# Optimization experiments

Hardware: AMD Instinct MI355X
Metric: run time of the kernel (lower is better)

The kernel has to match this reference:

```python
import jax, jax.numpy as jnp
import numpy as np

N_NODES = 50000
N_EDGES = 800000
F_IN, F_HID, F_OUT = 128, 64, 32


def setup_inputs() -> dict:
    key = jax.random.key(0)
    k1, k2, k3, k4, k5, k6 = jax.random.split(key, 6)
    x = jax.random.normal(k1, (N_NODES, F_IN), dtype=jnp.float32)
    edge_index = jax.random.randint(k2, (2, N_EDGES), 0, N_NODES, dtype=jnp.int64)
    # Glorot-ish init for the two GCNConv linear layers
    W1 = jax.random.normal(k3, (F_IN, F_HID), dtype=jnp.float32) / np.sqrt(F_IN)
    b1 = jnp.zeros((F_HID,), dtype=jnp.float32)
    W2 = jax.random.normal(k4, (F_HID, F_OUT), dtype=jnp.float32) / np.sqrt(F_HID)
    b2 = jnp.zeros((F_OUT,), dtype=jnp.float32)
    return {"x": x, "edge_index": edge_index, "W1": W1, "b1": b1, "W2": W2, "b2": b2}


def _gcn_conv(x, src, dst, norm, W, b):
    # GCNConv: linear transform, then D^{-1/2}(A+I)D^{-1/2} aggregation
    xw = x @ W                                # [N, F_out]
    msg = xw[src] * norm[:, None]             # [E+N, F_out] gather + scale
    out = jax.ops.segment_sum(msg, dst, num_segments=x.shape[0])
    return out + b


def reference(x, edge_index, W1, b1, W2, b2):
    n = x.shape[0]
    self_loops = jnp.arange(n, dtype=edge_index.dtype)
    src = jnp.concatenate([edge_index[0], self_loops])  # [E+N]
    dst = jnp.concatenate([edge_index[1], self_loops])
    # symmetric degree normalization (self-loops guarantee deg >= 1)
    deg = jax.ops.segment_sum(jnp.ones_like(dst, dtype=x.dtype), dst, num_segments=n)
    dinv = jax.lax.rsqrt(deg)
    norm = dinv[src] * dinv[dst]              # [E+N]

    h = _gcn_conv(x, src, dst, norm, W1, b1)
    h = jax.nn.relu(h)
    # dropout p=0.5 is identity in eval mode (training=False)
    out = _gcn_conv(h, src, dst, norm, W2, b2)
    return out
```

## Files before the change

kernel.cpp:

```cpp
#include <hip/hip_runtime.h>
#include <hip/hip_fp16.h>

#define NN 50000
#define NE 800000
#define F_IN 128
#define F_HID 64
#define F_OUT 32
#define CAP 48
#define NPB 196
#define EPB 4096
#define NB2 391
#define CELL 40
#define NXW1 782

typedef _Float16 f16x8 __attribute__((ext_vector_type(8)));
typedef float f32x4 __attribute__((ext_vector_type(4)));
#define XS_STR 136


__global__ __launch_bounds__(256) void fused_xw1_partition_kernel(
        const float* __restrict__ x, const float* __restrict__ W,
        const int* __restrict__ src, const int* __restrict__ dst,
        int* __restrict__ cnt2t, unsigned int* __restrict__ bstore2,
        __half* __restrict__ outh) {
    __shared__ _Float16 xs[64 * XS_STR];
    __shared__ _Float16 wt[64 * XS_STR];
    __shared__ int hist[4][NB2];
    __shared__ int cur[NB2];
    int t = threadIdx.x;

    if (blockIdx.x < NPB) {
        int blk = blockIdx.x;
        for (int i = t; i < 4 * NB2; i += 256) ((int*)hist)[i] = 0;
        __syncthreads();
        int wv = t >> 6;
        int base = blk * EPB;
        unsigned int pk[16];
#pragma unroll
        for (int i = 0; i < 16; ++i) {
            int e = base + i * 256 + t;
            if (e < NE) {
                unsigned int d = (unsigned int)dst[e];
                unsigned int s = (unsigned int)src[e];
                pk[i] = (d << 16) | s;
                atomicAdd(&hist[wv][d >> 7], 1);
            } else {
                pk[i] = 0xFFFFFFFFu;
            }
        }
        __syncthreads();
        for (int b = t; b < NB2; b += 256) {
            int h = hist[0][b] + hist[1][b] + hist[2][b] + hist[3][b];
            cur[b] = 0;
            cnt2t[b * NPB + blk] = h;
        }
        __syncthreads();
#pragma unroll
        for (int i = 0; i < 16; ++i) {
            unsigned int p = pk[i];
            if (p != 0xFFFFFFFFu) {
                int b = p >> 23;
                int pos = atomicAdd(&cur[b], 1);
                if (pos < CELL) bstore2[((size_t)blk * NB2 + b) * CELL + pos] = p;
            }
        }
        return;
    }

    int node0 = (blockIdx.x - NPB) * 64;

    {
        int r = t >> 2;
        int c0 = (t & 3) * 32;
        int gn = node0 + r;
        if (gn > NN - 1) gn = NN - 1;
        const float4* xrow = (const float4*)(x + (size_t)gn * F_IN);
#pragma unroll
        for (int i = 0; i < 8; ++i) {
            float4 v = xrow[(c0 >> 2) + i];
            _Float16* p = &xs[r * XS_STR + c0 + i * 4];
            p[0] = (_Float16)v.x; p[1] = (_Float16)v.y;
            p[2] = (_Float16)v.z; p[3] = (_Float16)v.w;
        }
    }
#pragma unroll
    for (int i = 0; i < 8; ++i) {
        int idx4 = t + i * 256;
        int k = idx4 >> 4;
        int n0 = (idx4 & 15) << 2;
        float4 v = ((const float4*)W)[idx4];
        wt[(n0 + 0) * XS_STR + k] = (_Float16)v.x;
        wt[(n0 + 1) * XS_STR + k] = (_Float16)v.y;
        wt[(n0 + 2) * XS_STR + k] = (_Float16)v.z;
        wt[(n0 + 3) * XS_STR + k] = (_Float16)v.w;
    }
    __syncthreads();

    int wave = t >> 6;
    int l = t & 63;
    int quad = l >> 4;
    int lm = l & 15;

    f32x4 acc[4] = {{0,0,0,0},{0,0,0,0},{0,0,0,0},{0,0,0,0}};
    const _Float16* abase = &xs[(wave * 16 + lm) * XS_STR + quad * 8];
#pragma unroll
    for (int kk4 = 0; kk4 < 4; ++kk4) {
        int kk = kk4 * 32;
        f16x8 a = *(const f16x8*)(abase + kk);
#pragma unroll
        for (int ft = 0; ft < 4; ++ft) {
            f16x8 b = *(const f16x8*)&wt[(ft * 16 + lm) * XS_STR + kk + quad * 8];
            acc[ft] = __builtin_amdgcn_mfma_f32_16x16x32_f16(a, b, acc[ft], 0, 0, 0);
        }
    }

    __syncthreads();
    _Float16* ot = xs;
#pragma unroll
    for (int ft = 0; ft < 4; ++ft) {
#pragma unroll
        for (int r = 0; r < 4; ++r) {
            int row_l = wave * 16 + quad * 4 + r;
            ot[row_l * 64 + ft * 16 + lm] = (_Float16)acc[ft][r];
        }
    }
    __syncthreads();
#pragma unroll
    for (int i = 0; i < 2; ++i) {
        int idx = t + i * 256;
        int row = idx >> 3;
        int c8 = (idx & 7) * 8;
        int gn = node0 + row;
        if (gn < NN)
            *(uint4*)(outh + (size_t)gn * 64 + c8) = *(const uint4*)&ot[row * 64 + c8];
    }
}


__device__ __forceinline__ void slot_insert(unsigned int p, int* cnt_l,
                                            unsigned short* slot_l) {
    int dl = (p >> 16) & 127;
    int pos = atomicAdd(&cnt_l[dl], 1);
    if (pos < CAP) slot_l[dl * CAP + pos] = (unsigned short)(p & 0xFFFFu);
}

__global__ __launch_bounds__(256) void build_slots_kernel(
        const int* __restrict__ cnt2t, const unsigned int* __restrict__ bstore2,
        unsigned short* __restrict__ slot, int* __restrict__ cnt_g, float* __restrict__ dinv) {
    __shared__ unsigned short slot_l[128 * CAP];
    __shared__ int cnt_l[128];
    int t = threadIdx.x;
    int b = blockIdx.x;
    if (t < 128) cnt_l[t] = 0;
    __syncthreads();

    if (t < NPB) {
        int blk = t;
        int c = cnt2t[b * NPB + blk];
        if (c > CELL) c = CELL;
        const uint4* seg4 = (const uint4*)(bstore2 + ((size_t)blk * NB2 + b) * CELL);
        int c4 = c >> 2;
        for (int q = 0; q < c4; ++q) {
            uint4 u = seg4[q];
            slot_insert(u.x, cnt_l, slot_l);
            slot_insert(u.y, cnt_l, slot_l);
            slot_insert(u.z, cnt_l, slot_l);
            slot_insert(u.w, cnt_l, slot_l);
        }
        const unsigned int* seg = (const unsigned int*)seg4;
        for (int j = c4 * 4; j < c; ++j) slot_insert(seg[j], cnt_l, slot_l);
    }
    __syncthreads();

    unsigned int* sg = (unsigned int*)(slot + (size_t)b * 128 * CAP);
    const unsigned int* sl = (const unsigned int*)slot_l;
    for (int j = t; j < 128 * CAP / 2; j += 256) sg[j] = sl[j];

    if (t < 128) {
        int n = b * 128 + t;
        if (n < NN) {
            int c = cnt_l[t];
            cnt_g[n] = c;
            dinv[n] = rsqrtf(1.0f + (float)c);
        }
    }
}


__global__ __launch_bounds__(256, 6) void gather64_w2_kernel(
        const __half* __restrict__ xw, const int* __restrict__ cnt,
        const unsigned short* __restrict__ slot, const float* __restrict__ dinv,
        const float* __restrict__ b1, const float* __restrict__ W2,
        __half* __restrict__ hw2h) {
    __shared__ float w2s[F_HID * F_OUT];
    __shared__ float hl[4][F_HID];
    int t = threadIdx.x;
    for (int i = t; i < F_HID * F_OUT / 4; i += 256)
        ((float4*)w2s)[i] = ((const float4*)W2)[i];
    __syncthreads();

    int lane = t & 63;
    int wv = t >> 6;
    int n = blockIdx.x * 4 + wv;
    int st = lane >> 4;
    int fl4 = lane & 15;
    const uint2* base = (const uint2*)xw;
    int deg = cnt[n];
    if (deg > CAP) deg = CAP;
    float din = dinv[n];
    const unsigned short* srow = slot + (size_t)n * CAP;
    uint2 u_self = base[(size_t)n * 16 + fl4];
    float4 bb = ((const float4*)b1)[fl4];
    float a0 = 0, a1 = 0, a2 = 0, a3 = 0;
    int e = st;
    for (; e + 12 < deg; e += 16) {
        int s0 = srow[e];
        int s1 = srow[e + 4];
        int s2 = srow[e + 8];
        int s3 = srow[e + 12];
        float dv0 = dinv[s0], dv1 = dinv[s1], dv2 = dinv[s2], dv3 = dinv[s3];
        uint2 u0 = base[(size_t)s0 * 16 + fl4];
        uint2 u1 = base[(size_t)s1 * 16 + fl4];
        uint2 u2 = base[(size_t)s2 * 16 + fl4];
        uint2 u3 = base[(size_t)s3 * 16 + fl4];
        float2 p0 = __half22float2(*(__half2*)&u0.x), p1 = __half22float2(*(__half2*)&u0.y);
        float2 q0 = __half22float2(*(__half2*)&u1.x), q1 = __half22float2(*(__half2*)&u1.y);
        float2 r0 = __half22float2(*(__half2*)&u2.x), r1 = __half22float2(*(__half2*)&u2.y);
        float2 t0 = __half22float2(*(__half2*)&u3.x), t1 = __half22float2(*(__half2*)&u3.y);
        a0 += dv0 * p0.x + dv1 * q0.x + dv2 * r0.x + dv3 * t0.x;
        a1 += dv0 * p0.y + dv1 * q0.y + dv2 * r0.y + dv3 * t0.y;
        a2 += dv0 * p1.x + dv1 * q1.x + dv2 * r1.x + dv3 * t1.x;
        a3 += dv0 * p1.y + dv1 * q1.y + dv2 * r1.y + dv3 * t1.y;
    }
    for (; e < deg; e += 4) {
        int s = srow[e];
        float dv = dinv[s];
        uint2 u = base[(size_t)s * 16 + fl4];
        float2 p0 = __half22float2(*(__half2*)&u.x);
        float2 p1 = __half22float2(*(__half2*)&u.y);
        a0 += dv * p0.x; a1 += dv * p0.y; a2 += dv * p1.x; a3 += dv * p1.y;
    }
    a0 += __shfl_xor(a0, 16, 64); a1 += __shfl_xor(a1, 16, 64);
    a2 += __shfl_xor(a2, 16, 64); a3 += __shfl_xor(a3, 16, 64);
    a0 += __shfl_xor(a0, 32, 64); a1 += __shfl_xor(a1, 32, 64);
    a2 += __shfl_xor(a2, 32, 64); a3 += __shfl_xor(a3, 32, 64);
    if (st == 0) {
        float2 s0 = __half22float2(*(__half2*)&u_self.x);
        float2 s1 = __half22float2(*(__half2*)&u_self.y);
        float v0 = din * (a0 + din * s0.x) + bb.x;
        float v1 = din * (a1 + din * s0.y) + bb.y;
        float v2 = din * (a2 + din * s1.x) + bb.z;
        float v3 = din * (a3 + din * s1.y) + bb.w;
        float* hr = &hl[wv][fl4 * 4];
        hr[0] = v0 > 0.f ? v0 : 0.f;
        hr[1] = v1 > 0.f ? v1 : 0.f;
        hr[2] = v2 > 0.f ? v2 : 0.f;
        hr[3] = v3 > 0.f ? v3 : 0.f;
    }
    asm volatile("s_waitcnt lgkmcnt(0)" ::: "memory");
    {
        int f = lane & 31;
        int kh = lane >> 5;
        const float* hr = &hl[wv][kh * 32];
        float acc = 0.0f;
#pragma unroll
        for (int k = 0; k < 32; ++k) acc += hr[k] * w2s[(kh * 32 + k) * F_OUT + f];
        acc += __shfl_xor(acc, 32, 64);
        if (kh == 0) hw2h[(size_t)n * F_OUT + f] = __float2half(acc * din);
    }
}


__global__ __launch_bounds__(256, 8) void gather32_kernel(
        const __half* __restrict__ scaled, const int* __restrict__ cnt,
        const unsigned short* __restrict__ slot, const float* __restrict__ dinv,
        const float* __restrict__ bias, float* __restrict__ out) {
    int lane = threadIdx.x & 63;
    int n = blockIdx.x * 4 + (threadIdx.x >> 6);
    if (n >= NN) return;
    int st = lane >> 3;
    int fl4 = lane & 7;
    const uint2* base = (const uint2*)scaled;
    int deg = cnt[n];
    if (deg > CAP) deg = CAP;
    const unsigned short* srow = slot + (size_t)n * CAP;
    uint2 u_self = base[(size_t)n * 8 + fl4];
    float4 b4 = ((const float4*)bias)[fl4];
    float a0 = 0, a1 = 0, a2 = 0, a3 = 0;
    int e = st;
    for (; e + 8 < deg; e += 16) {
        int s0 = srow[e];
        int s1 = srow[e + 8];
        uint2 u0 = base[(size_t)s0 * 8 + fl4];
        uint2 u1 = base[(size_t)s1 * 8 + fl4];
        float2 p0 = __half22float2(*(__half2*)&u0.x);
        float2 p1 = __half22float2(*(__half2*)&u0.y);
        float2 q0 = __half22float2(*(__half2*)&u1.x);
        float2 q1 = __half22float2(*(__half2*)&u1.y);
        a0 += p0.x + q0.x; a1 += p0.y + q0.y;
        a2 += p1.x + q1.x; a3 += p1.y + q1.y;
    }
    for (; e < deg; e += 8) {
        int s = srow[e];
        uint2 u = base[(size_t)s * 8 + fl4];
        float2 p0 = __half22float2(*(__half2*)&u.x);
        float2 p1 = __half22float2(*(__half2*)&u.y);
        a0 += p0.x; a1 += p0.y; a2 += p1.x; a3 += p1.y;
    }
    a0 += __shfl_xor(a0, 8, 64);  a1 += __shfl_xor(a1, 8, 64);
    a2 += __shfl_xor(a2, 8, 64);  a3 += __shfl_xor(a3, 8, 64);
    a0 += __shfl_xor(a0, 16, 64); a1 += __shfl_xor(a1, 16, 64);
    a2 += __shfl_xor(a2, 16, 64); a3 += __shfl_xor(a3, 16, 64);
    a0 += __shfl_xor(a0, 32, 64); a1 += __shfl_xor(a1, 32, 64);
    a2 += __shfl_xor(a2, 32, 64); a3 += __shfl_xor(a3, 32, 64);
    if (st == 0) {
        float2 s0 = __half22float2(*(__half2*)&u_self.x);
        float2 s1 = __half22float2(*(__half2*)&u_self.y);
        float di = dinv[n];
        float4 r;
        r.x = di * (a0 + s0.x) + b4.x;
        r.y = di * (a1 + s0.y) + b4.y;
        r.z = di * (a2 + s1.x) + b4.z;
        r.w = di * (a3 + s1.y) + b4.w;
        ((float4*)out)[(size_t)n * 8 + fl4] = r;
    }
}


extern "C" void kernel_launch(void* const* d_in, const int* in_sizes, int n_in,
                              void* d_out, int out_size, void* d_ws, size_t ws_size,
                              hipStream_t stream) {
    const float* x  = (const float*)d_in[0];
    const int*   ei = (const int*)d_in[1];
    const float* W1 = (const float*)d_in[2];
    const float* b1 = (const float*)d_in[3];
    const float* W2 = (const float*)d_in[4];
    const float* b2 = (const float*)d_in[5];
    const int* src = ei;
    const int* dst = ei + NE;

    float*          ws      = (float*)d_ws;
    float*          dinv    = ws;
    int*            cnt     = (int*)(ws + 50048);
    int*            cnt2t   = (int*)(ws + 100096);
    unsigned int*   bstore2 = (unsigned int*)(ws + 176768);
    unsigned short* slot    = (unsigned short*)(ws + 3242208);
    __half*         xw1h    = (__half*)(ws + 4443360);
    __half*         hw2h    = (__half*)(ws + 6043360);
    float*          out     = (float*)d_out;

    fused_xw1_partition_kernel<<<NPB + NXW1, 256, 0, stream>>>(
        x, W1, src, dst, cnt2t, bstore2, xw1h);
    build_slots_kernel<<<NB2, 256, 0, stream>>>(cnt2t, bstore2, slot, cnt, dinv);
    gather64_w2_kernel<<<NN / 4, 256, 0, stream>>>(xw1h, cnt, slot, dinv, b1, W2, hw2h);
    gather32_kernel<<<NN / 4, 256, 0, stream>>>(hw2h, cnt, slot, dinv, b2, out);
}
```

Measured before the change: 149.1 us.

## Move X·W1 GEMM into slot-building kernel and hoist gather loads ahead of degree

The dense X·W1 GEMM blocks now launch alongside the slot-building blocks instead of the partition blocks, so the partition kernel becomes a small standalone launch. Both layers' gather kernels issue their first batch of neighbour indices and feature loads before reading the degree. They then mask out-of-range lanes, unrolling two fixed rounds before a remainder loop. This aims to raise memory-level parallelism and shorten dependency chains, at the cost of speculative reads of unused slot entries and a shared-memory union in the fused kernel.

```diff
diff --git a/kernel.cpp b/kernel.cpp
--- a/kernel.cpp
+++ b/kernel.cpp
@@ -18,56 +18,108 @@
 #define XS_STR 136
 
 
-__global__ __launch_bounds__(256) void fused_xw1_partition_kernel(
-        const float* __restrict__ x, const float* __restrict__ W,
+__global__ __launch_bounds__(256) void partition_kernel(
         const int* __restrict__ src, const int* __restrict__ dst,
-        int* __restrict__ cnt2t, unsigned int* __restrict__ bstore2,
-        __half* __restrict__ outh) {
-    __shared__ _Float16 xs[64 * XS_STR];
-    __shared__ _Float16 wt[64 * XS_STR];
+        int* __restrict__ cnt2t, unsigned int* __restrict__ bstore2) {
     __shared__ int hist[4][NB2];
     __shared__ int cur[NB2];
     int t = threadIdx.x;
-
-    if (blockIdx.x < NPB) {
-        int blk = blockIdx.x;
-        for (int i = t; i < 4 * NB2; i += 256) ((int*)hist)[i] = 0;
+    int blk = blockIdx.x;
+    for (int i = t; i < 4 * NB2; i += 256) ((int*)hist)[i] = 0;
+    __syncthreads();
+    int wv = t >> 6;
+    int base = blk * EPB;
+    unsigned int pk[16];
+#pragma unroll
+    for (int i = 0; i < 16; ++i) {
+        int e = base + i * 256 + t;
+        if (e < NE) {
+            unsigned int d = (unsigned int)dst[e];
+            unsigned int s = (unsigned int)src[e];
+            pk[i] = (d << 16) | s;
+            atomicAdd(&hist[wv][d >> 7], 1);
+        } else {
+            pk[i] = 0xFFFFFFFFu;
+        }
+    }
+    __syncthreads();
+    for (int b = t; b < NB2; b += 256) {
+        int h = hist[0][b] + hist[1][b] + hist[2][b] + hist[3][b];
+        cur[b] = 0;
+        cnt2t[b * NPB + blk] = h;
+    }
+    __syncthreads();
+#pragma unroll
+    for (int i = 0; i < 16; ++i) {
+        unsigned int p = pk[i];
+        if (p != 0xFFFFFFFFu) {
+            int b = p >> 23;
+            int pos = atomicAdd(&cur[b], 1);
+            if (pos < CELL) bstore2[((size_t)blk * NB2 + b) * CELL + pos] = p;
+        }
+    }
+}
+
+
+__device__ __forceinline__ void slot_insert(unsigned int p, int* cnt_l,
+                                            unsigned short* slot_l) {
+    int dl = (p >> 16) & 127;
+    int pos = atomicAdd(&cnt_l[dl], 1);
+    if (pos < CAP) slot_l[dl * CAP + pos] = (unsigned short)(p & 0xFFFFu);
+}
+
+__global__ __launch_bounds__(256) void fused_slots_xw1_kernel(
+        const int* __restrict__ cnt2t, const unsigned int* __restrict__ bstore2,
+        unsigned short* __restrict__ slot, int* __restrict__ cnt_g,
+        float* __restrict__ dinv,
+        const float* __restrict__ x, const float* __restrict__ W,
+        __half* __restrict__ outh) {
+    __shared__ __align__(16) char smem[64 * XS_STR * 2 * sizeof(_Float16)];
+    int t = threadIdx.x;
+
+    if (blockIdx.x < NB2) {
+        unsigned short* slot_l = (unsigned short*)smem;
+        int* cnt_l = (int*)(smem + 128 * CAP * sizeof(unsigned short));
+        int b = blockIdx.x;
+        if (t < 128) cnt_l[t] = 0;
         __syncthreads();
-        int wv = t >> 6;
-        int base = blk * EPB;
-        unsigned int pk[16];
-#pragma unroll
-        for (int i = 0; i < 16; ++i) {
-            int e = base + i * 256 + t;
-            if (e < NE) {
-                unsigned int d = (unsigned int)dst[e];
-                unsigned int s = (unsigned int)src[e];
-                pk[i] = (d << 16) | s;
-                atomicAdd(&hist[wv][d >> 7], 1);
-            } else {
-                pk[i] = 0xFFFFFFFFu;
+
+        if (t < NPB) {
+            int blk = t;
+            int c = cnt2t[b * NPB + blk];
+            if (c > CELL) c = CELL;
+            const uint4* seg4 = (const uint4*)(bstore2 + ((size_t)blk * NB2 + b) * CELL);
+            int c4 = c >> 2;
+            for (int q = 0; q < c4; ++q) {
+                uint4 u = seg4[q];
+                slot_insert(u.x, cnt_l, slot_l);
+                slot_insert(u.y, cnt_l, slot_l);
+                slot_insert(u.z, cnt_l, slot_l);
+                slot_insert(u.w, cnt_l, slot_l);
             }
+            const unsigned int* seg = (const unsigned int*)seg4;
+            for (int j = c4 * 4; j < c; ++j) slot_insert(seg[j], cnt_l, slot_l);
         }
         __syncthreads();
-        for (int b = t; b < NB2; b += 256) {
-            int h = hist[0][b] + hist[1][b] + hist[2][b] + hist[3][b];
-            cur[b] = 0;
-            cnt2t[b * NPB + blk] = h;
-        }
-        __syncthreads();
-#pragma unroll
-        for (int i = 0; i < 16; ++i) {
-            unsigned int p = pk[i];
-            if (p != 0xFFFFFFFFu) {
-                int b = p >> 23;
-                int pos = atomicAdd(&cur[b], 1);
-                if (pos < CELL) bstore2[((size_t)blk * NB2 + b) * CELL + pos] = p;
+
+        unsigned int* sg = (unsigned int*)(slot + (size_t)b * 128 * CAP);
+        const unsigned int* sl = (const unsigned int*)slot_l;
+        for (int j = t; j < 128 * CAP / 2; j += 256) sg[j] = sl[j];
+
+        if (t < 128) {
+            int n = b * 128 + t;
+            if (n < NN) {
+                int c = cnt_l[t];
+                cnt_g[n] = c;
+                dinv[n] = rsqrtf(1.0f + (float)c);
             }
         }
         return;
     }
 
-    int node0 = (blockIdx.x - NPB) * 64;
+    _Float16* xs = (_Float16*)smem;
+    _Float16* wt = xs + 64 * XS_STR;
+    int node0 = (blockIdx.x - NB2) * 64;
 
     {
         int r = t >> 2;
@@ -133,56 +185,6 @@
         int gn = node0 + row;
         if (gn < NN)
             *(uint4*)(outh + (size_t)gn * 64 + c8) = *(const uint4*)&ot[row * 64 + c8];
-    }
-}
-
-
-__device__ __forceinline__ void slot_insert(unsigned int p, int* cnt_l,
-                                            unsigned short* slot_l) {
-    int dl = (p >> 16) & 127;
-    int pos = atomicAdd(&cnt_l[dl], 1);
-    if (pos < CAP) slot_l[dl * CAP + pos] = (unsigned short)(p & 0xFFFFu);
-}
-
-__global__ __launch_bounds__(256) void build_slots_kernel(
-        const int* __restrict__ cnt2t, const unsigned int* __restrict__ bstore2,
-        unsigned short* __restrict__ slot, int* __restrict__ cnt_g, float* __restrict__ dinv) {
-    __shared__ unsigned short slot_l[128 * CAP];
-    __shared__ int cnt_l[128];
-    int t = threadIdx.x;
-    int b = blockIdx.x;
-    if (t < 128) cnt_l[t] = 0;
-    __syncthreads();
-
-    if (t < NPB) {
-        int blk = t;
-        int c = cnt2t[b * NPB + blk];
-        if (c > CELL) c = CELL;
-        const uint4* seg4 = (const uint4*)(bstore2 + ((size_t)blk * NB2 + b) * CELL);
-        int c4 = c >> 2;
-        for (int q = 0; q < c4; ++q) {
-            uint4 u = seg4[q];
-            slot_insert(u.x, cnt_l, slot_l);
-            slot_insert(u.y, cnt_l, slot_l);
-            slot_insert(u.z, cnt_l, slot_l);
-            slot_insert(u.w, cnt_l, slot_l);
-        }
-        const unsigned int* seg = (const unsigned int*)seg4;
-        for (int j = c4 * 4; j < c; ++j) slot_insert(seg[j], cnt_l, slot_l);
-    }
-    __syncthreads();
-
-    unsigned int* sg = (unsigned int*)(slot + (size_t)b * 128 * CAP);
-    const unsigned int* sl = (const unsigned int*)slot_l;
-    for (int j = t; j < 128 * CAP / 2; j += 256) sg[j] = sl[j];
-
-    if (t < 128) {
-        int n = b * 128 + t;
-        if (n < NN) {
-            int c = cnt_l[t];
-            cnt_g[n] = c;
-            dinv[n] = rsqrtf(1.0f + (float)c);
-        }
     }
 }
 
@@ -205,52 +207,81 @@
     int st = lane >> 4;
     int fl4 = lane & 15;
     const uint2* base = (const uint2*)xw;
+    const unsigned short* srow = slot + (size_t)n * CAP;
+    int s0 = srow[st];
+    int s1 = srow[st + 4];
+    int s2 = srow[st + 8];
+    int s3 = srow[st + 12];
+    uint2 u_self = base[(size_t)n * 16 + fl4];
+    float4 bb = ((const float4*)b1)[fl4];
     int deg = cnt[n];
     if (deg > CAP) deg = CAP;
     float din = dinv[n];
-    const unsigned short* srow = slot + (size_t)n * CAP;
-    uint2 u_self = base[(size_t)n * 16 + fl4];
-    float4 bb = ((const float4*)b1)[fl4];
-    float a0 = 0, a1 = 0, a2 = 0, a3 = 0;
-    int e = st;
-    for (; e + 12 < deg; e += 16) {
-        int s0 = srow[e];
-        int s1 = srow[e + 4];
-        int s2 = srow[e + 8];
-        int s3 = srow[e + 12];
-        float dv0 = dinv[s0], dv1 = dinv[s1], dv2 = dinv[s2], dv3 = dinv[s3];
-        uint2 u0 = base[(size_t)s0 * 16 + fl4];
-        uint2 u1 = base[(size_t)s1 * 16 + fl4];
-        uint2 u2 = base[(size_t)s2 * 16 + fl4];
-        uint2 u3 = base[(size_t)s3 * 16 + fl4];
-        float2 p0 = __half22float2(*(__half2*)&u0.x), p1 = __half22float2(*(__half2*)&u0.y);
-        float2 q0 = __half22float2(*(__half2*)&u1.x), q1 = __half22float2(*(__half2*)&u1.y);
-        float2 r0 = __half22float2(*(__half2*)&u2.x), r1 = __half22float2(*(__half2*)&u2.y);
-        float2 t0 = __half22float2(*(__half2*)&u3.x), t1 = __half22float2(*(__half2*)&u3.y);
+    uint2 u0 = base[(size_t)s0 * 16 + fl4];
+    uint2 u1 = base[(size_t)s1 * 16 + fl4];
+    uint2 u2 = base[(size_t)s2 * 16 + fl4];
+    uint2 u3 = base[(size_t)s3 * 16 + fl4];
+    float dv0 = (st      < deg) ? dinv[s0] : 0.f;
+    float dv1 = (st + 4  < deg) ? dinv[s1] : 0.f;
+    float dv2 = (st + 8  < deg) ? dinv[s2] : 0.f;
+    float dv3 = (st + 12 < deg) ? dinv[s3] : 0.f;
+    if (st      >= deg) { u0.x = 0u; u0.y = 0u; }
+    if (st + 4  >= deg) { u1.x = 0u; u1.y = 0u; }
+    if (st + 8  >= deg) { u2.x = 0u; u2.y = 0u; }
+    if (st + 12 >= deg) { u3.x = 0u; u3.y = 0u; }
+    float2 p0 = __half22float2(*(__half2*)&u0.x), p1 = __half22float2(*(__half2*)&u0.y);
+    float2 q0 = __half22float2(*(__half2*)&u1.x), q1 = __half22float2(*(__half2*)&u1.y);
+    float2 r0 = __half22float2(*(__half2*)&u2.x), r1 = __half22float2(*(__half2*)&u2.y);
+    float2 t0 = __half22float2(*(__half2*)&u3.x), t1 = __half22float2(*(__half2*)&u3.y);
+    float a0 = dv0 * p0.x + dv1 * q0.x + dv2 * r0.x + dv3 * t0.x;
+    float a1 = dv0 * p0.y + dv1 * q0.y + dv2 * r0.y + dv3 * t0.y;
+    float a2 = dv0 * p1.x + dv1 * q1.x + dv2 * r1.x + dv3 * t1.x;
+    float a3 = dv0 * p1.y + dv1 * q1.y + dv2 * r1.y + dv3 * t1.y;
+    if (deg > 16) {
+        s0 = srow[st + 16];
+        s1 = srow[st + 20];
+        s2 = srow[st + 24];
+        s3 = srow[st + 28];
+        u0 = base[(size_t)s0 * 16 + fl4];
+        u1 = base[(size_t)s1 * 16 + fl4];
+        u2 = base[(size_t)s2 * 16 + fl4];
+        u3 = base[(size_t)s3 * 16 + fl4];
+        dv0 = (st + 16 < deg) ? dinv[s0] : 0.f;
+        dv1 = (st + 20 < deg) ? dinv[s1] : 0.f;
+        dv2 = (st + 24 < deg) ? dinv[s2] : 0.f;
+        dv3 = (st + 28 < deg) ? dinv[s3] : 0.f;
+        if (st + 16 >= deg) { u0.x = 0u; u0.y = 0u; }
+        if (st + 20 >= deg) { u1.x = 0u; u1.y = 0u; }
+        if (st + 24 >= deg) { u2.x = 0u; u2.y = 0u; }
+        if (st + 28 >= deg) { u3.x = 0u; u3.y = 0u; }
+        p0 = __half22float2(*(__half2*)&u0.x); p1 = __half22float2(*(__half2*)&u0.y);
+        q0 = __half22float2(*(__half2*)&u1.x); q1 = __half22float2(*(__half2*)&u1.y);
+        r0 = __half22float2(*(__half2*)&u2.x); r1 = __half22float2(*(__half2*)&u2.y);
+        t0 = __half22float2(*(__half2*)&u3.x); t1 = __half22float2(*(__half2*)&u3.y);
         a0 += dv0 * p0.x + dv1 * q0.x + dv2 * r0.x + dv3 * t0.x;
         a1 += dv0 * p0.y + dv1 * q0.y + dv2 * r0.y + dv3 * t0.y;
         a2 += dv0 * p1.x + dv1 * q1.x + dv2 * r1.x + dv3 * t1.x;
         a3 += dv0 * p1.y + dv1 * q1.y + dv2 * r1.y + dv3 * t1.y;
     }
-    for (; e < deg; e += 4) {
+    for (int e = st + 32; e < deg; e += 4) {
         int s = srow[e];
         float dv = dinv[s];
         uint2 u = base[(size_t)s * 16 + fl4];
-        float2 p0 = __half22float2(*(__half2*)&u.x);
-        float2 p1 = __half22float2(*(__half2*)&u.y);
-        a0 += dv * p0.x; a1 += dv * p0.y; a2 += dv * p1.x; a3 += dv * p1.y;
+        float2 w0 = __half22float2(*(__half2*)&u.x);
+        float2 w1 = __half22float2(*(__half2*)&u.y);
+        a0 += dv * w0.x; a1 += dv * w0.y; a2 += dv * w1.x; a3 += dv * w1.y;
     }
     a0 += __shfl_xor(a0, 16, 64); a1 += __shfl_xor(a1, 16, 64);
     a2 += __shfl_xor(a2, 16, 64); a3 += __shfl_xor(a3, 16, 64);
     a0 += __shfl_xor(a0, 32, 64); a1 += __shfl_xor(a1, 32, 64);
     a2 += __shfl_xor(a2, 32, 64); a3 += __shfl_xor(a3, 32, 64);
     if (st == 0) {
-        float2 s0 = __half22float2(*(__half2*)&u_self.x);
-        float2 s1 = __half22float2(*(__half2*)&u_self.y);
-        float v0 = din * (a0 + din * s0.x) + bb.x;
-        float v1 = din * (a1 + din * s0.y) + bb.y;
-        float v2 = din * (a2 + din * s1.x) + bb.z;
-        float v3 = din * (a3 + din * s1.y) + bb.w;
+        float2 s0f = __half22float2(*(__half2*)&u_self.x);
+        float2 s1f = __half22float2(*(__half2*)&u_self.y);
+        float v0 = din * (a0 + din * s0f.x) + bb.x;
+        float v1 = din * (a1 + din * s0f.y) + bb.y;
+        float v2 = din * (a2 + din * s1f.x) + bb.z;
+        float v3 = din * (a3 + din * s1f.y) + bb.w;
         float* hr = &hl[wv][fl4 * 4];
         hr[0] = v0 > 0.f ? v0 : 0.f;
         hr[1] = v1 > 0.f ? v1 : 0.f;
@@ -281,31 +312,44 @@
     int st = lane >> 3;
     int fl4 = lane & 7;
     const uint2* base = (const uint2*)scaled;
+    const unsigned short* srow = slot + (size_t)n * CAP;
+    int s0 = srow[st];
+    int s1 = srow[st + 8];
+    uint2 u_self = base[(size_t)n * 8 + fl4];
+    float4 b4 = ((const float4*)bias)[fl4];
     int deg = cnt[n];
     if (deg > CAP) deg = CAP;
-    const unsigned short* srow = slot + (size_t)n * CAP;
-    uint2 u_self = base[(size_t)n * 8 + fl4];
-    float4 b4 = ((const float4*)bias)[fl4];
-    float a0 = 0, a1 = 0, a2 = 0, a3 = 0;
-    int e = st;
-    for (; e + 8 < deg; e += 16) {
-        int s0 = srow[e];
-        int s1 = srow[e + 8];
-        uint2 u0 = base[(size_t)s0 * 8 + fl4];
-        uint2 u1 = base[(size_t)s1 * 8 + fl4];
-        float2 p0 = __half22float2(*(__half2*)&u0.x);
-        float2 p1 = __half22float2(*(__half2*)&u0.y);
-        float2 q0 = __half22float2(*(__half2*)&u1.x);
-        float2 q1 = __half22float2(*(__half2*)&u1.y);
+    float di = dinv[n];
+    uint2 u0 = base[(size_t)s0 * 8 + fl4];
+    uint2 u1 = base[(size_t)s1 * 8 + fl4];
+    if (st     >= deg) { u0.x = 0u; u0.y = 0u; }
+    if (st + 8 >= deg) { u1.x = 0u; u1.y = 0u; }
+    float2 p0 = __half22float2(*(__half2*)&u0.x);
+    float2 p1 = __half22float2(*(__half2*)&u0.y);
+    float2 q0 = __half22float2(*(__half2*)&u1.x);
+    float2 q1 = __half22float2(*(__half2*)&u1.y);
+    float a0 = p0.x + q0.x, a1 = p0.y + q0.y;
+    float a2 = p1.x + q1.x, a3 = p1.y + q1.y;
+    if (deg > 16) {
+        s0 = srow[st + 16];
+        s1 = srow[st + 24];
+        u0 = base[(size_t)s0 * 8 + fl4];
+        u1 = base[(size_t)s1 * 8 + fl4];
+        if (st + 16 >= deg) { u0.x = 0u; u0.y = 0u; }
+        if (st + 24 >= deg) { u1.x = 0u; u1.y = 0u; }
+        p0 = __half22float2(*(__half2*)&u0.x);
+        p1 = __half22float2(*(__half2*)&u0.y);
+        q0 = __half22float2(*(__half2*)&u1.x);
+        q1 = __half22float2(*(__half2*)&u1.y);
         a0 += p0.x + q0.x; a1 += p0.y + q0.y;
         a2 += p1.x + q1.x; a3 += p1.y + q1.y;
     }
-    for (; e < deg; e += 8) {
+    for (int e = st + 32; e < deg; e += 8) {
         int s = srow[e];
         uint2 u = base[(size_t)s * 8 + fl4];
-        float2 p0 = __half22float2(*(__half2*)&u.x);
-        float2 p1 = __half22float2(*(__half2*)&u.y);
-        a0 += p0.x; a1 += p0.y; a2 += p1.x; a3 += p1.y;
+        float2 w0 = __half22float2(*(__half2*)&u.x);
+        float2 w1 = __half22float2(*(__half2*)&u.y);
+        a0 += w0.x; a1 += w0.y; a2 += w1.x; a3 += w1.y;
     }
     a0 += __shfl_xor(a0, 8, 64);  a1 += __shfl_xor(a1, 8, 64);
     a2 += __shfl_xor(a2, 8, 64);  a3 += __shfl_xor(a3, 8, 64);
@@ -314,14 +358,13 @@
     a0 += __shfl_xor(a0, 32, 64); a1 += __shfl_xor(a1, 32, 64);
     a2 += __shfl_xor(a2, 32, 64); a3 += __shfl_xor(a3, 32, 64);
     if (st == 0) {
-        float2 s0 = __half22float2(*(__half2*)&u_self.x);
-        float2 s1 = __half22float2(*(__half2*)&u_self.y);
-        float di = dinv[n];
+        float2 s0f = __half22float2(*(__half2*)&u_self.x);
+        float2 s1f = __half22float2(*(__half2*)&u_self.y);
         float4 r;
-        r.x = di * (a0 + s0.x) + b4.x;
-        r.y = di * (a1 + s0.y) + b4.y;
-        r.z = di * (a2 + s1.x) + b4.z;
-        r.w = di * (a3 + s1.y) + b4.w;
+        r.x = di * (a0 + s0f.x) + b4.x;
+        r.y = di * (a1 + s0f.y) + b4.y;
+        r.z = di * (a2 + s1f.x) + b4.z;
+        r.w = di * (a3 + s1f.y) + b4.w;
         ((float4*)out)[(size_t)n * 8 + fl4] = r;
     }
 }
@@ -349,9 +392,9 @@
     __half*         hw2h    = (__half*)(ws + 6043360);
     float*          out     = (float*)d_out;
 
-    fused_xw1_partition_kernel<<<NPB + NXW1, 256, 0, stream>>>(
-        x, W1, src, dst, cnt2t, bstore2, xw1h);
-    build_slots_kernel<<<NB2, 256, 0, stream>>>(cnt2t, bstore2, slot, cnt, dinv);
+    partition_kernel<<<NPB, 256, 0, stream>>>(src, dst, cnt2t, bstore2);
+    fused_slots_xw1_kernel<<<NB2 + NXW1, 256, 0, stream>>>(
+        cnt2t, bstore2, slot, cnt, dinv, x, W1, xw1h);
     gather64_w2_kernel<<<NN / 4, 256, 0, stream>>>(xw1h, cnt, slot, dinv, b1, W2, hw2h);
     gather32_kernel<<<NN / 4, 256, 0, stream>>>(hw2h, cnt, slot, dinv, b2, out);
 }
```

Result: faster. 144.0 us (-3.4%).
